# Performance work log

Hardware: AMD Instinct MI355X
Metric: run time of the kernel (lower is better)

The kernel has to match this reference:

```python
import jax, jax.numpy as jnp
import numpy as np

B, T, D_IN, H, L, D_OUT = 128, 1024, 256, 512, 2, 128


def setup_inputs() -> dict:
    key = jax.random.key(0)
    ks = jax.random.split(key, 11)
    s = lambda fan: 1.0 / np.sqrt(H)
    inp = {"x": jax.random.normal(ks[0], (B, T, D_IN), dtype=jnp.float32)}
    dims = [D_IN, H]
    for l in range(L):
        d = dims[l]
        inp[f"W_ih{l}"] = jax.random.uniform(ks[1 + 4 * l], (4 * H, d), minval=-s(d), maxval=s(d), dtype=jnp.float32)
        inp[f"W_hh{l}"] = jax.random.uniform(ks[2 + 4 * l], (4 * H, H), minval=-s(H), maxval=s(H), dtype=jnp.float32)
        inp[f"b_ih{l}"] = jax.random.uniform(ks[3 + 4 * l], (4 * H,), minval=-s(H), maxval=s(H), dtype=jnp.float32)
        inp[f"b_hh{l}"] = jax.random.uniform(ks[4 + 4 * l], (4 * H,), minval=-s(H), maxval=s(H), dtype=jnp.float32)
    inp["fc_w"] = jax.random.uniform(ks[9], (D_OUT, H), minval=-s(H), maxval=s(H), dtype=jnp.float32)
    inp["fc_b"] = jax.random.uniform(ks[10], (D_OUT,), minval=-s(H), maxval=s(H), dtype=jnp.float32)
    return inp


def _cell(x_t, h, c, W_ih, W_hh, b_ih, b_hh):
    # gates: [B, 4H], torch LSTMCell order i, f, g, o
    gates = x_t @ W_ih.T + b_ih + h @ W_hh.T + b_hh
    i, f, g, o = jnp.split(gates, 4, axis=-1)
    c_new = jax.nn.sigmoid(f) * c + jax.nn.sigmoid(i) * jnp.tanh(g)
    h_new = jax.nn.sigmoid(o) * jnp.tanh(c_new)
    return h_new, c_new


def reference(x, W_ih0, W_hh0, b_ih0, b_hh0, W_ih1, W_hh1, b_ih1, b_hh1, fc_w, fc_b):
    params = [(W_ih0, W_hh0, b_ih0, b_hh0), (W_ih1, W_hh1, b_ih1, b_hh1)]
    B_ = x.shape[0]
    h0 = tuple(jnp.zeros((B_, H), x.dtype) for _ in range(L))
    c0 = tuple(jnp.zeros((B_, H), x.dtype) for _ in range(L))

    def step(carry, x_t):
        hs, cs = carry
        new_h, new_c = [], []
        inp = x_t
        for l in range(L):
            hn, cn = _cell(inp, hs[l], cs[l], *params[l])
            new_h.append(hn)
            new_c.append(cn)
            inp = hn
        return (tuple(new_h), tuple(new_c)), None

    (hs, _), _ = jax.lax.scan(step, (h0, c0), jnp.swapaxes(x, 0, 1))
    return hs[-1] @ fc_w.T + fc_b
```

## Files before the change

### kernel.cpp

```cpp
#include <hip/hip_runtime.h>

#define B_   128
#define T_   1024
#define DIN  256
#define H_   512
#define DOUT 128
#define NWG  256

typedef __attribute__((ext_vector_type(4))) float f32x4;
typedef __attribute__((ext_vector_type(8))) short bf16x8;
typedef __attribute__((ext_vector_type(4))) short bf16x4;

#define H0_OFF   0u
#define H1_OFF   (256u << 10)
#define FIN_OFF  (512u << 10)
#define FLG_OFF  (768u << 10)
#define XB_OFF   (800u << 10)
#define XB_BYTES ((size_t)T_ * 32 * 128 * 8 * 2)

__device__ __forceinline__ short f2bf(float f) {
  union { float f; unsigned u; } v; v.f = f;
  unsigned r = v.u + 0x7FFFu + ((v.u >> 16) & 1u);
  return (short)(r >> 16);
}
__device__ __forceinline__ float sigf(float x) { return 1.f / (1.f + __expf(-x)); }

__device__ __forceinline__ void st_bf(short* p, short v) {
  __hip_atomic_store((unsigned short*)p, (unsigned short)v,
                     __ATOMIC_RELAXED, __HIP_MEMORY_SCOPE_AGENT);
}
__device__ __forceinline__ void st_f32(float* p, float v) {
  __hip_atomic_store(p, v, __ATOMIC_RELAXED, __HIP_MEMORY_SCOPE_AGENT);
}
__device__ __forceinline__ void st_u32(unsigned* p, unsigned v) {
  __hip_atomic_store(p, v, __ATOMIC_RELAXED, __HIP_MEMORY_SCOPE_AGENT);
}
__device__ __forceinline__ unsigned ld_u32(const unsigned* p) {
  return __hip_atomic_load(p, __ATOMIC_RELAXED, __HIP_MEMORY_SCOPE_AGENT);
}
__device__ __forceinline__ void ld16(bf16x8& d, const short* p) {
  asm volatile("global_load_dwordx4 %0, %1, off sc0 sc1" : "=v"(d) : "v"(p));
}

__global__ void lstm_init_kernel(void* ws) {
  int gid = blockIdx.x * blockDim.x + threadIdx.x;
  unsigned* p = (unsigned*)ws;
  __hip_atomic_store(p + gid, 0u, __ATOMIC_RELAXED, __HIP_MEMORY_SCOPE_AGENT);
  if (gid < 8192) {
    unsigned* f = (unsigned*)((char*)ws + FLG_OFF);
    __hip_atomic_store(f + gid, 0u, __ATOMIC_RELAXED, __HIP_MEMORY_SCOPE_AGENT);
  }
}

__global__ void xconv_kernel(const float* __restrict__ x, short* __restrict__ xb) {
  int blk = blockIdx.x;
  int t = blk >> 5, g = blk & 31;
  int b = threadIdx.x >> 1, hf = (threadIdx.x & 1) * 4;
  f32x4 v = *(const f32x4*)(x + ((size_t)b * T_ + t) * DIN + g * 8 + hf);
  bf16x4 o;
#pragma unroll
  for (int j = 0; j < 4; ++j) o[j] = f2bf(v[j]);
  *(bf16x4*)(xb + ((size_t)(t * 32 + g) * 128 + b) * 8 + hf) = o;
}

__global__ __launch_bounds__(256, 1) void lstm_coop_kernel(
    const float* __restrict__ x,
    const float* __restrict__ wih0, const float* __restrict__ whh0,
    const float* __restrict__ bih0, const float* __restrict__ bhh0,
    const float* __restrict__ wih1, const float* __restrict__ whh1,
    const float* __restrict__ bih1, const float* __restrict__ bhh1,
    const float* __restrict__ fcw,  const float* __restrict__ fcb,
    const short* __restrict__ xb,
    void* __restrict__ ws, float* __restrict__ out)
{
  __shared__ short sWih0[16][264];
  __shared__ short sWhh0[16][520];
  __shared__ short sWih1[16][520];
  __shared__ short sWhh1[16][520];

  const int tid  = threadIdx.x;
  const int wg   = blockIdx.x;
  const int cgid = wg >> 1;
  const int bh   = wg & 1;
  const int j0   = cgid * 4;

  char* wsb = (char*)ws;
  short* h0buf = (short*)(wsb + H0_OFF);
  short* h1buf = (short*)(wsb + H1_OFF);
  float* h1fin = (float*)(wsb + FIN_OFF);
  unsigned* flags = (unsigned*)(wsb + FLG_OFF);
  unsigned* ownf  = flags + wg * 32;

  for (int idx = tid; idx < 16 * DIN; idx += 256) {
    int lr = idx >> 8, k = idx & 255;
    int grow = (lr & 3) * H_ + j0 + (lr >> 2);
    sWih0[lr][k] = f2bf(wih0[(size_t)grow * DIN + k]);
  }
  for (int idx = tid; idx < 16 * H_; idx += 256) {
    int lr = idx >> 9, k = idx & 511;
    int grow = (lr & 3) * H_ + j0 + (lr >> 2);
    sWhh0[lr][k] = f2bf(whh0[(size_t)grow * H_ + k]);
    sWih1[lr][k] = f2bf(wih1[(size_t)grow * H_ + k]);
    sWhh1[lr][k] = f2bf(whh1[(size_t)grow * H_ + k]);
  }
  __syncthreads();

  const int lane = tid & 63;
  const int wid  = tid >> 6;
  const int ln   = lane & 15;
  const int q    = lane >> 4;
  const int b    = bh * 64 + wid * 16 + ln;
  const int jj   = j0 + q;
  const int hwof = (jj >> 3) * 1024 + (jj & 7);

  float bias0[4], bias1[4];
#pragma unroll
  for (int g = 0; g < 4; ++g) {
    int rr = g * H_ + j0 + q;
    bias0[g] = bih0[rr] + bhh0[rr];
    bias1[g] = bih1[rr] + bhh1[rr];
  }

  bf16x8 xp[8];
  auto xpref = [&](int t) {
    if (xb) {
      const short* p = xb + ((size_t)(t * 32 + q) * 128 + b) * 8;
#pragma unroll
      for (int ks = 0; ks < 8; ++ks) xp[ks] = *(const bf16x8*)(p + ks * 4096);
    } else {
      const float* xrow = x + ((size_t)b * T_ + t) * DIN + q * 8;
#pragma unroll
      for (int ks = 0; ks < 8; ++ks) {
        f32x4 xa = *(const f32x4*)(xrow + ks * 32);
        f32x4 xc = *(const f32x4*)(xrow + ks * 32 + 4);
#pragma unroll
        for (int j = 0; j < 4; ++j) { xp[ks][j] = f2bf(xa[j]); xp[ks][4 + j] = f2bf(xc[j]); }
      }
    }
  };
  xpref(0);

  float c0v = 0.f, c1v = 0.f;

  for (int r = 0; r <= T_; ++r) {
    const short* h0rd = h0buf + (r & 1) * 65536;
    short*       h0wr = h0buf + ((r + 1) & 1) * 65536;
    const short* h1rd = h1buf + (r & 1) * 65536;
    short*       h1wr = h1buf + ((r + 1) & 1) * 65536;

    bf16x8 f0[16], f1[16];
    {
      const short* p0 = h0rd + q * 1024 + (size_t)b * 8;
      const short* p1 = h1rd + q * 1024 + (size_t)b * 8;
#pragma unroll
      for (int ks = 0; ks < 16; ++ks) ld16(f0[ks], p0 + ks * 4096);
#pragma unroll
      for (int ks = 0; ks < 16; ++ks) ld16(f1[ks], p1 + ks * 4096);
      asm volatile("s_waitcnt vmcnt(0)" ::: "memory");
      __builtin_amdgcn_sched_barrier(0);
    }

    if (r < T_) {
      f32x4 accA, accB;
      accA[0] = bias0[0]; accA[1] = bias0[1]; accA[2] = bias0[2]; accA[3] = bias0[3];
      accB[0] = 0.f; accB[1] = 0.f; accB[2] = 0.f; accB[3] = 0.f;
#pragma unroll
      for (int ks = 0; ks < 8; ++ks) {
        bf16x8 af = *(const bf16x8*)(&sWih0[ln][ks * 32 + q * 8]);
        if (ks & 1) accB = __builtin_amdgcn_mfma_f32_16x16x32_bf16(af, xp[ks], accB, 0, 0, 0);
        else        accA = __builtin_amdgcn_mfma_f32_16x16x32_bf16(af, xp[ks], accA, 0, 0, 0);
      }
#pragma unroll
      for (int ks = 0; ks < 16; ++ks) {
        bf16x8 af = *(const bf16x8*)(&sWhh0[ln][ks * 32 + q * 8]);
        if (ks & 1) accB = __builtin_amdgcn_mfma_f32_16x16x32_bf16(af, f0[ks], accB, 0, 0, 0);
        else        accA = __builtin_amdgcn_mfma_f32_16x16x32_bf16(af, f0[ks], accA, 0, 0, 0);
      }
      f32x4 acc = accA + accB;
      float ig = sigf(acc[0]), fg = sigf(acc[1]), gg = tanhf(acc[2]), og = sigf(acc[3]);
      float cn = fg * c0v + ig * gg;
      c0v = cn;
      st_bf(h0wr + hwof + (size_t)b * 8, f2bf(og * tanhf(cn)));
    }

    if (r >= 1) {
      f32x4 accA, accB;
      accA[0] = bias1[0]; accA[1] = bias1[1]; accA[2] = bias1[2]; accA[3] = bias1[3];
      accB[0] = 0.f; accB[1] = 0.f; accB[2] = 0.f; accB[3] = 0.f;
#pragma unroll
      for (int ks = 0; ks < 16; ++ks) {
        bf16x8 af = *(const bf16x8*)(&sWih1[ln][ks * 32 + q * 8]);
        if (ks & 1) accB = __builtin_amdgcn_mfma_f32_16x16x32_bf16(af, f0[ks], accB, 0, 0, 0);
        else        accA = __builtin_amdgcn_mfma_f32_16x16x32_bf16(af, f0[ks], accA, 0, 0, 0);
      }
#pragma unroll
      for (int ks = 0; ks < 16; ++ks) {
        bf16x8 af = *(const bf16x8*)(&sWhh1[ln][ks * 32 + q * 8]);
        if (ks & 1) accB = __builtin_amdgcn_mfma_f32_16x16x32_bf16(af, f1[ks], accB, 0, 0, 0);
        else        accA = __builtin_amdgcn_mfma_f32_16x16x32_bf16(af, f1[ks], accA, 0, 0, 0);
      }
      f32x4 acc = accA + accB;
      float ig = sigf(acc[0]), fg = sigf(acc[1]), gg = tanhf(acc[2]), og = sigf(acc[3]);
      float cn = fg * c1v + ig * gg;
      c1v = cn;
      float hn = og * tanhf(cn);
      st_bf(h1wr + hwof + (size_t)b * 8, f2bf(hn));
      if (r == T_) st_f32(h1fin + (size_t)b * H_ + jj, hn);
    }

    asm volatile("s_waitcnt vmcnt(0)" ::: "memory");
    __syncthreads();
    if (tid == 0) st_u32(ownf, (unsigned)(r + 1));
    if (r + 1 < T_) xpref(r + 1);
    {
      const unsigned R = (unsigned)(r + 1);
      const unsigned* fl = flags + ((((tid & 127) << 1) | bh) << 5);
      while (ld_u32(fl) < R) __builtin_amdgcn_s_sleep(1);
    }
    __syncthreads();
    asm volatile("" ::: "memory");
  }

  {
    const unsigned R = (unsigned)(T_ + 1);
    const unsigned* fl = flags + ((((tid & 127) << 1) | (bh ^ 1)) << 5);
    while (ld_u32(fl) < R) __builtin_amdgcn_s_sleep(1);
  }
  __syncthreads();
  asm volatile("" ::: "memory");

  if (wg < B_ && tid < DOUT) {
    const float* hrow = h1fin + (size_t)wg * H_;
    const float* wrow = fcw + (size_t)tid * H_;
    float a = fcb[tid];
    for (int j = 0; j < H_; j += 2) {
      union { unsigned long long q; float f[2]; } c;
      c.q = __hip_atomic_load((const unsigned long long*)(hrow + j),
                              __ATOMIC_RELAXED, __HIP_MEMORY_SCOPE_AGENT);
      a += c.f[0] * wrow[j] + c.f[1] * wrow[j + 1];
    }
    out[(size_t)wg * DOUT + tid] = a;
  }
}

extern "C" void kernel_launch(void* const* d_in, const int* in_sizes, int n_in,
                              void* d_out, int out_size, void* d_ws, size_t ws_size,
                              hipStream_t stream) {
  const float* x    = (const float*)d_in[0];
  const float* wih0 = (const float*)d_in[1];
  const float* whh0 = (const float*)d_in[2];
  const float* bih0 = (const float*)d_in[3];
  const float* bhh0 = (const float*)d_in[4];
  const float* wih1 = (const float*)d_in[5];
  const float* whh1 = (const float*)d_in[6];
  const float* bih1 = (const float*)d_in[7];
  const float* bhh1 = (const float*)d_in[8];
  const float* fcw  = (const float*)d_in[9];
  const float* fcb  = (const float*)d_in[10];
  float* out = (float*)d_out;

  char* wsb = (char*)d_ws;
  bool use_xb = ws_size >= (size_t)XB_OFF + XB_BYTES;
  short* xbw = use_xb ? (short*)(wsb + XB_OFF) : nullptr;
  const short* xb = xbw;

  hipLaunchKernelGGL(lstm_init_kernel, dim3(512), dim3(256), 0, stream, d_ws);
  if (use_xb)
    hipLaunchKernelGGL(xconv_kernel, dim3(T_ * 32), dim3(256), 0, stream, x, xbw);

  void* args[] = { (void*)&x, (void*)&wih0, (void*)&whh0, (void*)&bih0, (void*)&bhh0,
                   (void*)&wih1, (void*)&whh1, (void*)&bih1, (void*)&bhh1,
                   (void*)&fcw, (void*)&fcb, (void*)&xb, (void*)&d_ws, (void*)&out };
  hipLaunchCooperativeKernel((const void*)lstm_coop_kernel,
                             dim3(NWG), dim3(256), args, 0, stream);
}
```

Measured before the change: 4.486 ms.

## Split K across waves with LDS reduction and keep weight fragments in registers

Each wave now covers a quarter of the K dimension for all 64 batch rows of the workgroup instead of the full K for 16 rows. Partial gate sums are reduced through shared memory before the activations. Weight fragments are loaded once into registers, removing per-step LDS reads of the weights. Each step now issues 4 independent MFMA chains per wave for better issue overlap, at the cost of extra __syncthreads and LDS traffic for the reduction. Launch bounds are changed to allow 2 workgroups per CU.

```diff
diff --git a/kernel.cpp b/kernel.cpp
--- a/kernel.cpp
+++ b/kernel.cpp
@@ -63,7 +63,7 @@
   *(bf16x4*)(xb + ((size_t)(t * 32 + g) * 128 + b) * 8 + hf) = o;
 }
 
-__global__ __launch_bounds__(256, 1) void lstm_coop_kernel(
+__global__ __launch_bounds__(256, 2) void lstm_coop_kernel(
     const float* __restrict__ x,
     const float* __restrict__ wih0, const float* __restrict__ whh0,
     const float* __restrict__ bih0, const float* __restrict__ bhh0,
@@ -77,6 +77,7 @@
   __shared__ short sWhh0[16][520];
   __shared__ short sWih1[16][520];
   __shared__ short sWhh1[16][520];
+  __shared__ f32x4 sred[4][4][64];
 
   const int tid  = threadIdx.x;
   const int wg   = blockIdx.x;
@@ -106,35 +107,50 @@
   __syncthreads();
 
   const int lane = tid & 63;
-  const int wid  = tid >> 6;
+  const int w    = tid >> 6;
   const int ln   = lane & 15;
   const int q    = lane >> 4;
-  const int b    = bh * 64 + wid * 16 + ln;
+  const int b    = bh * 64 + w * 16 + ln;
   const int jj   = j0 + q;
   const int hwof = (jj >> 3) * 1024 + (jj & 7);
 
-  float bias0[4], bias1[4];
+  bf16x8 aIH0[2], aHH0[4], aIH1[4], aHH1[4];
+#pragma unroll
+  for (int s2 = 0; s2 < 2; ++s2)
+    aIH0[s2] = *(const bf16x8*)(&sWih0[ln][(2 * w + s2) * 32 + q * 8]);
+#pragma unroll
+  for (int s = 0; s < 4; ++s) {
+    aHH0[s] = *(const bf16x8*)(&sWhh0[ln][(4 * w + s) * 32 + q * 8]);
+    aIH1[s] = *(const bf16x8*)(&sWih1[ln][(4 * w + s) * 32 + q * 8]);
+    aHH1[s] = *(const bf16x8*)(&sWhh1[ln][(4 * w + s) * 32 + q * 8]);
+  }
+
+  f32x4 bias0v, bias1v;
 #pragma unroll
   for (int g = 0; g < 4; ++g) {
-    int rr = g * H_ + j0 + q;
-    bias0[g] = bih0[rr] + bhh0[rr];
-    bias1[g] = bih1[rr] + bhh1[rr];
-  }
-
-  bf16x8 xp[8];
+    int rr = g * H_ + jj;
+    bias0v[g] = bih0[rr] + bhh0[rr];
+    bias1v[g] = bih1[rr] + bhh1[rr];
+  }
+
+  bf16x8 xp[2][4];
   auto xpref = [&](int t) {
-    if (xb) {
-      const short* p = xb + ((size_t)(t * 32 + q) * 128 + b) * 8;
-#pragma unroll
-      for (int ks = 0; ks < 8; ++ks) xp[ks] = *(const bf16x8*)(p + ks * 4096);
-    } else {
-      const float* xrow = x + ((size_t)b * T_ + t) * DIN + q * 8;
-#pragma unroll
-      for (int ks = 0; ks < 8; ++ks) {
-        f32x4 xa = *(const f32x4*)(xrow + ks * 32);
-        f32x4 xc = *(const f32x4*)(xrow + ks * 32 + 4);
-#pragma unroll
-        for (int j = 0; j < 4; ++j) { xp[ks][j] = f2bf(xa[j]); xp[ks][4 + j] = f2bf(xc[j]); }
+#pragma unroll
+    for (int s2 = 0; s2 < 2; ++s2) {
+      const int g = q + 4 * (2 * w + s2);
+#pragma unroll
+      for (int bt = 0; bt < 4; ++bt) {
+        const int bb = bh * 64 + bt * 16 + ln;
+        if (xb) {
+          xp[s2][bt] = *(const bf16x8*)(xb + ((size_t)(t * 32 + g) * 128 + bb) * 8);
+        } else {
+          const float* p = x + ((size_t)bb * T_ + t) * DIN + (2 * w + s2) * 32 + q * 8;
+          f32x4 a = *(const f32x4*)p, b2 = *(const f32x4*)(p + 4);
+          bf16x8 f;
+#pragma unroll
+          for (int j = 0; j < 4; ++j) { f[j] = f2bf(a[j]); f[4 + j] = f2bf(b2[j]); }
+          xp[s2][bt] = f;
+        }
       }
     }
   };
@@ -148,60 +164,62 @@
     const short* h1rd = h1buf + (r & 1) * 65536;
     short*       h1wr = h1buf + ((r + 1) & 1) * 65536;
 
-    bf16x8 f0[16], f1[16];
-    {
-      const short* p0 = h0rd + q * 1024 + (size_t)b * 8;
-      const short* p1 = h1rd + q * 1024 + (size_t)b * 8;
-#pragma unroll
-      for (int ks = 0; ks < 16; ++ks) ld16(f0[ks], p0 + ks * 4096);
-#pragma unroll
-      for (int ks = 0; ks < 16; ++ks) ld16(f1[ks], p1 + ks * 4096);
-      asm volatile("s_waitcnt vmcnt(0)" ::: "memory");
-      __builtin_amdgcn_sched_barrier(0);
-    }
-
+    bf16x8 f0[4][4], f1[4][4];
+#pragma unroll
+    for (int bt = 0; bt < 4; ++bt) {
+      const int bb = bh * 64 + bt * 16 + ln;
+      const short* pb0 = h0rd + (size_t)bb * 8;
+      const short* pb1 = h1rd + (size_t)bb * 8;
+#pragma unroll
+      for (int s = 0; s < 4; ++s) {
+        const int g = q + 4 * (4 * w + s);
+        ld16(f0[bt][s], pb0 + g * 1024);
+        ld16(f1[bt][s], pb1 + g * 1024);
+      }
+    }
+    asm volatile("s_waitcnt vmcnt(0)" ::: "memory");
+    __builtin_amdgcn_sched_barrier(0);
+
+    f32x4 p0[4], p1[4];
+#pragma unroll
+    for (int bt = 0; bt < 4; ++bt)
+#pragma unroll
+      for (int g = 0; g < 4; ++g) { p0[bt][g] = 0.f; p1[bt][g] = 0.f; }
+#pragma unroll
+    for (int s2 = 0; s2 < 2; ++s2)
+#pragma unroll
+      for (int bt = 0; bt < 4; ++bt)
+        p0[bt] = __builtin_amdgcn_mfma_f32_16x16x32_bf16(aIH0[s2], xp[s2][bt], p0[bt], 0, 0, 0);
+#pragma unroll
+    for (int s = 0; s < 4; ++s)
+#pragma unroll
+      for (int bt = 0; bt < 4; ++bt) {
+        p0[bt] = __builtin_amdgcn_mfma_f32_16x16x32_bf16(aHH0[s], f0[bt][s], p0[bt], 0, 0, 0);
+        p1[bt] = __builtin_amdgcn_mfma_f32_16x16x32_bf16(aIH1[s], f0[bt][s], p1[bt], 0, 0, 0);
+        p1[bt] = __builtin_amdgcn_mfma_f32_16x16x32_bf16(aHH1[s], f1[bt][s], p1[bt], 0, 0, 0);
+      }
+
+#pragma unroll
+    for (int bt = 0; bt < 4; ++bt) sred[w][bt][lane] = p0[bt];
+    __syncthreads();
     if (r < T_) {
-      f32x4 accA, accB;
-      accA[0] = bias0[0]; accA[1] = bias0[1]; accA[2] = bias0[2]; accA[3] = bias0[3];
-      accB[0] = 0.f; accB[1] = 0.f; accB[2] = 0.f; accB[3] = 0.f;
-#pragma unroll
-      for (int ks = 0; ks < 8; ++ks) {
-        bf16x8 af = *(const bf16x8*)(&sWih0[ln][ks * 32 + q * 8]);
-        if (ks & 1) accB = __builtin_amdgcn_mfma_f32_16x16x32_bf16(af, xp[ks], accB, 0, 0, 0);
-        else        accA = __builtin_amdgcn_mfma_f32_16x16x32_bf16(af, xp[ks], accA, 0, 0, 0);
-      }
-#pragma unroll
-      for (int ks = 0; ks < 16; ++ks) {
-        bf16x8 af = *(const bf16x8*)(&sWhh0[ln][ks * 32 + q * 8]);
-        if (ks & 1) accB = __builtin_amdgcn_mfma_f32_16x16x32_bf16(af, f0[ks], accB, 0, 0, 0);
-        else        accA = __builtin_amdgcn_mfma_f32_16x16x32_bf16(af, f0[ks], accA, 0, 0, 0);
-      }
-      f32x4 acc = accA + accB;
-      float ig = sigf(acc[0]), fg = sigf(acc[1]), gg = tanhf(acc[2]), og = sigf(acc[3]);
-      float cn = fg * c0v + ig * gg;
+      f32x4 s = sred[0][w][lane] + sred[1][w][lane]
+              + sred[2][w][lane] + sred[3][w][lane] + bias0v;
+      float ig = sigf(s[0]), fg = sigf(s[1]), g2 = tanhf(s[2]), og = sigf(s[3]);
+      float cn = fg * c0v + ig * g2;
       c0v = cn;
       st_bf(h0wr + hwof + (size_t)b * 8, f2bf(og * tanhf(cn)));
     }
-
+    __syncthreads();
+
+#pragma unroll
+    for (int bt = 0; bt < 4; ++bt) sred[w][bt][lane] = p1[bt];
+    __syncthreads();
     if (r >= 1) {
-      f32x4 accA, accB;
-      accA[0] = bias1[0]; accA[1] = bias1[1]; accA[2] = bias1[2]; accA[3] = bias1[3];
-      accB[0] = 0.f; accB[1] = 0.f; accB[2] = 0.f; accB[3] = 0.f;
-#pragma unroll
-      for (int ks = 0; ks < 16; ++ks) {
-        bf16x8 af = *(const bf16x8*)(&sWih1[ln][ks * 32 + q * 8]);
-        if (ks & 1) accB = __builtin_amdgcn_mfma_f32_16x16x32_bf16(af, f0[ks], accB, 0, 0, 0);
-        else        accA = __builtin_amdgcn_mfma_f32_16x16x32_bf16(af, f0[ks], accA, 0, 0, 0);
-      }
-#pragma unroll
-      for (int ks = 0; ks < 16; ++ks) {
-        bf16x8 af = *(const bf16x8*)(&sWhh1[ln][ks * 32 + q * 8]);
-        if (ks & 1) accB = __builtin_amdgcn_mfma_f32_16x16x32_bf16(af, f1[ks], accB, 0, 0, 0);
-        else        accA = __builtin_amdgcn_mfma_f32_16x16x32_bf16(af, f1[ks], accA, 0, 0, 0);
-      }
-      f32x4 acc = accA + accB;
-      float ig = sigf(acc[0]), fg = sigf(acc[1]), gg = tanhf(acc[2]), og = sigf(acc[3]);
-      float cn = fg * c1v + ig * gg;
+      f32x4 s = sred[0][w][lane] + sred[1][w][lane]
+              + sred[2][w][lane] + sred[3][w][lane] + bias1v;
+      float ig = sigf(s[0]), fg = sigf(s[1]), g2 = tanhf(s[2]), og = sigf(s[3]);
+      float cn = fg * c1v + ig * g2;
       c1v = cn;
       float hn = og * tanhf(cn);
       st_bf(h1wr + hwof + (size_t)b * 8, f2bf(hn));
```

New measurement: 7.244 ms. 61.5% more time.
